# Kernel optimization log

Measured on AMD Instinct MI355X. Metric: run time of the kernel, lower is better.

## Reference

```python
import jax, jax.numpy as jnp
import numpy as np

BN_EPS = 1e-5


def ball_query(pos, radius, k):
    """PointNet++-style ball query: for each point, the first k point indices
    (in index order) whose distance < radius; shorter lists are padded with the
    first valid index (self is always valid since dist=0). pos: (b,n,3).
    Returns idx: (b,n,k) int32."""
    b, n, _ = pos.shape
    sq = jnp.sum(pos * pos, axis=-1)                       # (b,n)
    d2 = sq[:, :, None] + sq[:, None, :] - 2.0 * jnp.einsum('bnc,bmc->bnm', pos, pos)
    mask = d2 < radius * radius                            # (b,n,n)
    cand = jnp.where(mask, jnp.arange(n, dtype=jnp.int32)[None, None, :], jnp.int32(n))
    # smallest-k indices in ascending order == first-k valid in index order
    neg_top, _ = jax.lax.top_k(-cand, k)                   # (b,n,k)
    idx = -neg_top
    first = idx[..., :1]
    idx = jnp.where(idx == n, first, idx)                  # pad with first neighbor
    return idx


def reference(pos, x, w1, gamma, beta, w2, b2, radius, k):
    pos = jax.lax.stop_gradient(pos)
    idx = ball_query(pos, radius, k)                       # (b,n,k)
    grouped = jax.vmap(lambda p, i: p[i])(pos, idx)        # (b,n,k,3)
    rel = grouped - pos[:, :, None, :]                     # center-subtract
    # 1x1 conv (3->3, no bias)
    h = jnp.einsum('bnkc,dc->bnkd', rel, w1)
    # BatchNorm2d (training-mode batch stats over b,k,n per channel)
    mean = jnp.mean(h, axis=(0, 1, 2))
    var = jnp.mean((h - mean) ** 2, axis=(0, 1, 2))
    h = (h - mean) * jax.lax.rsqrt(var + BN_EPS) * gamma + beta
    h = jax.nn.relu(h)
    # 1x1 conv (3->out_channel) + bias
    pe = jnp.einsum('bnkd,ed->bnke', h, w2) + b2           # (b,n,k,C)
    pe = jnp.max(pe, axis=2)                               # max over k neighbors
    return x + pe


def setup_inputs() -> dict:
    key = jax.random.key(0)
    ks = jax.random.split(key, 5)
    b, n, c, kk = 2, 8192, 64, 32
    pos = jax.random.uniform(ks[0], (b, n, 3), dtype=jnp.float32)
    x = jax.random.normal(ks[1], (b, n, c), dtype=jnp.float32)
    w1 = jax.random.normal(ks[2], (3, 3), dtype=jnp.float32) * 0.5
    gamma = jnp.ones((3,), dtype=jnp.float32)
    beta = jnp.zeros((3,), dtype=jnp.float32)
    w2 = jax.random.normal(ks[3], (c, 3), dtype=jnp.float32) * 0.5
    b2 = jnp.zeros((c,), dtype=jnp.float32)
    radius = jnp.float32(0.1)
    return {"pos": pos, "x": x, "w1": w1, "gamma": gamma, "beta": beta,
            "w2": w2, "b2": b2, "radius": radius, "k": kk}
```

## Files before the change

kernel.cpp:

```cpp
#include <hip/hip_runtime.h>
#include <math.h>

#define NPTS   8192
#define NBATCH 2
#define NQ     (NPTS * NBATCH)
#define KNB    32
#define CFEAT  64
#define BN_EPS 1e-5f

#define MAXC     1000
#define CSTR     1024
#define CAP_HIT  128
#define CAP_CAND 640

#define QBK2  16
#define NBLK2 (NQ / QBK2)

#define WS_H    0
#define WS_PART (NQ * 3 * KNB)
#define WS_CS   (WS_PART + 6 * NBLK2)
#define WS_BIN  (WS_CS + 2 * CSTR)

__device__ __forceinline__ int grid_from_r(double rd) {
    int G = (int)(1.0 / rd);
    if (G < 1) G = 1;
    while (G > 1 && 1.0 / (double)G < rd) --G;
    if (G > 10) G = 10;
    return G;
}

__device__ __forceinline__ int mbcnt64(unsigned long long m) {
    return (int)__builtin_amdgcn_mbcnt_hi((unsigned)(m >> 32),
             __builtin_amdgcn_mbcnt_lo((unsigned)m, 0u));
}

__global__ __launch_bounds__(256) void kA_bin(
    const float* __restrict__ pos, const float* __restrict__ radius,
    float* __restrict__ ws)
{
    __shared__ int hist[MAXC];
    __shared__ int offs[MAXC + 1];
    __shared__ int cur[MAXC];
    __shared__ int scan[256];

    const int tid = threadIdx.x;
    const int batch = blockIdx.x;
    const float* bpos = pos + (size_t)batch * NPTS * 3;
    const double rd = (double)radius[0];
    const int G = grid_from_r(rd);
    const float Gf = (float)G;
    const int NC = G * G * G;

    for (int c = tid; c < NC; c += 256) hist[c] = 0;
    __syncthreads();
    for (int p = tid; p < NPTS; p += 256) {
        float x = bpos[p * 3], y = bpos[p * 3 + 1], z = bpos[p * 3 + 2];
        int cx = min((int)(x * Gf), G - 1);
        int cy = min((int)(y * Gf), G - 1);
        int cz = min((int)(z * Gf), G - 1);
        atomicAdd(&hist[(cz * G + cy) * G + cx], 1);
    }
    __syncthreads();

    const int CH = (MAXC + 255) / 256;
    const int base = tid * CH;
    int s = 0;
#pragma unroll
    for (int i = 0; i < CH; ++i) { int c = base + i; s += (c < NC) ? hist[c] : 0; }
    scan[tid] = s;
    __syncthreads();
    for (int off = 1; off < 256; off <<= 1) {
        int v = (tid >= off) ? scan[tid - off] : 0;
        __syncthreads();
        scan[tid] += v;
        __syncthreads();
    }
    int excl = (tid > 0) ? scan[tid - 1] : 0;
#pragma unroll
    for (int i = 0; i < CH; ++i) {
        int c = base + i;
        if (c < NC) { offs[c] = excl; excl += hist[c]; }
    }
    if (tid == 0) offs[NC] = NPTS;
    __syncthreads();
    for (int c = tid; c < NC; c += 256) cur[c] = offs[c];
    int* cs = (int*)ws + WS_CS + batch * CSTR;
    for (int c = tid; c <= NC; c += 256) cs[c] = offs[c];
    __syncthreads();

    float4* bin = (float4*)(ws + WS_BIN) + (size_t)batch * NPTS;
    for (int p = tid; p < NPTS; p += 256) {
        float x = bpos[p * 3], y = bpos[p * 3 + 1], z = bpos[p * 3 + 2];
        int cx = min((int)(x * Gf), G - 1);
        int cy = min((int)(y * Gf), G - 1);
        int cz = min((int)(z * Gf), G - 1);
        int slot = atomicAdd(&cur[(cz * G + cy) * G + cx], 1);
        bin[slot] = make_float4(x, y, z, __int_as_float(p));
    }
}

__global__ __launch_bounds__(256) void k2_query(
    const float* __restrict__ pos, const float* __restrict__ w1,
    const float* __restrict__ radius, float* __restrict__ ws)
{
    __shared__ int   candl[4][CAP_CAND];
    __shared__ int   hitl[QBK2][CAP_HIT];
    __shared__ int   seli[4][KNB];
    __shared__ float sred[4][6];

    const int tid = threadIdx.x, lane = tid & 63, wave = tid >> 6;
    const int qbase = blockIdx.x * QBK2;
    const int batch = qbase / NPTS;
    const float* bpos = pos + (size_t)batch * NPTS * 3;
    const double rd  = (double)radius[0];
    const double r2d = rd * rd;
    const int G = grid_from_r(rd);
    const float Gf = (float)G;
    const int* cs = (const int*)ws + WS_CS + batch * CSTR;
    const float4* bin = (const float4*)(ws + WS_BIN) + (size_t)batch * NPTS;

    float w1r[9];
#pragma unroll
    for (int i = 0; i < 9; ++i) w1r[i] = w1[i];

    float ls0 = 0.f, ls1 = 0.f, ls2 = 0.f;
    float lq0 = 0.f, lq1 = 0.f, lq2 = 0.f;

    for (int q = 0; q < 4; ++q) {
        const int qg = qbase + wave * 4 + q;
        const int ql = qg - batch * NPTS;
        const float qx = bpos[ql * 3], qy = bpos[ql * 3 + 1], qz = bpos[ql * 3 + 2];
        const double qxd = (double)qx, qyd = (double)qy, qzd = (double)qz;
        const double qsd = fma(qzd, qzd, fma(qyd, qyd, qxd * qxd));
        const int cx = min((int)(qx * Gf), G - 1);
        const int cy = min((int)(qy * Gf), G - 1);
        const int cz = min((int)(qz * Gf), G - 1);

        int cnt_l = 0, start_l = 0;
        if (lane < 27) {
            int dx = lane % 3 - 1, dy = (lane / 3) % 3 - 1, dz = lane / 9 - 1;
            int nx = cx + dx, ny = cy + dy, nz = cz + dz;
            if (nx >= 0 && nx < G && ny >= 0 && ny < G && nz >= 0 && nz < G) {
                int c = (nz * G + ny) * G + nx;
                start_l = cs[c];
                cnt_l = cs[c + 1] - start_l;
            }
        }
        int incl = cnt_l;
#pragma unroll
        for (int off = 1; off < 32; off <<= 1) {
            int v = __shfl_up(incl, off);
            if (lane >= off) incl += v;
        }
        int T = __shfl(incl, 26);
        if (T > CAP_CAND) T = CAP_CAND;
        const int pref = incl - cnt_l;
        if (lane < 27) {
            for (int t = 0; t < cnt_l; ++t) {
                int d = pref + t;
                if (d < CAP_CAND) candl[wave][d] = start_l + t;
            }
        }

        const int qs = wave * 4 + q;
        int hc = 0;
        for (int b0 = 0; b0 < T; b0 += 64) {
            int ss = b0 + lane;
            bool act = ss < T;
            int slot = act ? candl[wave][ss] : 0;
            float4 P = bin[slot];
            double xj = (double)P.x, yj = (double)P.y, zj = (double)P.z;
            double sqj = fma(zj, zj, fma(yj, yj, xj * xj));
            double dot = fma(zj, qzd, fma(yj, qyd, xj * qxd));
            double dd  = (qsd + sqj) - 2.0 * dot;
            bool in = act && (dd < r2d);
            unsigned long long bal = __ballot(in);
            if (in) {
                int p2 = hc + mbcnt64(bal);
                if (p2 < CAP_HIT) hitl[qs][p2] = __float_as_int(P.w);
            }
            hc += (int)__popcll(bal);
        }
        if (hc > CAP_HIT) hc = CAP_HIT;

        if (hc <= KNB) {
            int v = (lane < hc) ? hitl[qs][lane] : 0x7FFFFFFF;
            int mn = v;
#pragma unroll
            for (int off = 32; off; off >>= 1) mn = min(mn, __shfl_xor(mn, off));
            if (lane < KNB) seli[wave][lane] = (lane < hc) ? v : mn;
        } else {
            int a = (lane < hc) ? hitl[qs][lane] : 0x7FFFFFFF;
            int b = (64 + lane < hc) ? hitl[qs][64 + lane] : 0x7FFFFFFF;
            int lo = 0, hi = NPTS - 1;
            while (lo < hi) {
                int mid = (lo + hi) >> 1;
                int c1 = (int)__popcll(__ballot(a <= mid)) +
                         (int)__popcll(__ballot(b <= mid));
                if (c1 >= KNB) hi = mid; else lo = mid + 1;
            }
            const int t = lo;
            unsigned long long ba = __ballot(a <= t);
            unsigned long long bb = __ballot(b <= t);
            int na = (int)__popcll(ba);
            if (a <= t) seli[wave][mbcnt64(ba)] = a;
            if (b <= t) seli[wave][na + mbcnt64(bb)] = b;
        }

        if (lane < KNB) {
            int j = seli[wave][lane];
            const float* pj = bpos + (size_t)j * 3;
            float rx = __fsub_rn(pj[0], qx);
            float ry = __fsub_rn(pj[1], qy);
            float rz = __fsub_rn(pj[2], qz);
            float h0 = fmaf(rz, w1r[2], fmaf(ry, w1r[1], __fmul_rn(rx, w1r[0])));
            float h1 = fmaf(rz, w1r[5], fmaf(ry, w1r[4], __fmul_rn(rx, w1r[3])));
            float h2 = fmaf(rz, w1r[8], fmaf(ry, w1r[7], __fmul_rn(rx, w1r[6])));
            float* hout = ws + WS_H + (size_t)qg * 3 * KNB;
            hout[0 * KNB + lane] = h0;
            hout[1 * KNB + lane] = h1;
            hout[2 * KNB + lane] = h2;
            ls0 += h0; ls1 += h1; ls2 += h2;
            lq0 += h0 * h0; lq1 += h1 * h1; lq2 += h2 * h2;
        }
    }

#pragma unroll
    for (int m = 1; m < 64; m <<= 1) {
        ls0 += __shfl_xor(ls0, m); ls1 += __shfl_xor(ls1, m); ls2 += __shfl_xor(ls2, m);
        lq0 += __shfl_xor(lq0, m); lq1 += __shfl_xor(lq1, m); lq2 += __shfl_xor(lq2, m);
    }
    if (lane == 0) {
        sred[wave][0] = ls0; sred[wave][1] = ls1; sred[wave][2] = ls2;
        sred[wave][3] = lq0; sred[wave][4] = lq1; sred[wave][5] = lq2;
    }
    __syncthreads();
    if (tid == 0) {
#pragma unroll
        for (int c = 0; c < 6; ++c) {
            float s = sred[0][c] + sred[1][c] + sred[2][c] + sred[3][c];
            ws[WS_PART + c * NBLK2 + blockIdx.x] = s;
        }
    }
}

__global__ __launch_bounds__(256) void k3_mlp(
    const float* __restrict__ ws, const float* __restrict__ gamma,
    const float* __restrict__ beta, const float* __restrict__ w2,
    const float* __restrict__ b2, const float* __restrict__ x,
    float* __restrict__ out)
{
    __shared__ float wred[4][6];
    __shared__ float sstat[6];
    __shared__ float g[4][KNB][3];

    const int tid = threadIdx.x, lane = tid & 63, wave = tid >> 6;

#pragma unroll
    for (int c = 0; c < 6; ++c) {
        float s = 0.f;
        for (int i = tid; i < NBLK2; i += 256) s += ws[WS_PART + c * NBLK2 + i];
#pragma unroll
        for (int m = 1; m < 64; m <<= 1) s += __shfl_xor(s, m);
        if (lane == 0) wred[wave][c] = s;
    }
    __syncthreads();
    if (tid < 3) {
        const double N = (double)((long long)NQ * KNB);
        double s = 0.0, sq = 0.0;
#pragma unroll
        for (int w = 0; w < 4; ++w) { s += wred[w][tid]; sq += wred[w][3 + tid]; }
        double mean = s / N;
        double var  = sq / N - mean * mean;
        sstat[tid]     = (float)mean;
        sstat[3 + tid] = (float)(1.0 / sqrt(var + (double)BN_EPS));
    }
    __syncthreads();

    const float m0 = sstat[0], m1 = sstat[1], m2 = sstat[2];
    const float i0 = sstat[3], i1 = sstat[4], i2 = sstat[5];
    const float g0c = gamma[0], g1c = gamma[1], g2c = gamma[2];
    const float b0c = beta[0],  b1c = beta[1],  b2c = beta[2];
    const float w20 = w2[lane * 3 + 0];
    const float w21 = w2[lane * 3 + 1];
    const float w22 = w2[lane * 3 + 2];
    const float bias = b2[lane];

    const int qg0 = blockIdx.x * QBK2 + wave * 4;
#pragma unroll
    for (int q = 0; q < 4; ++q) {
        const int qg = qg0 + q;
        if (lane < KNB) {
            const float* hin = ws + WS_H + (size_t)qg * 3 * KNB;
            float h0 = hin[0 * KNB + lane];
            float h1 = hin[1 * KNB + lane];
            float h2 = hin[2 * KNB + lane];
            float n0 = __fadd_rn(__fmul_rn(__fmul_rn(__fsub_rn(h0, m0), i0), g0c), b0c);
            float n1 = __fadd_rn(__fmul_rn(__fmul_rn(__fsub_rn(h1, m1), i1), g1c), b1c);
            float n2 = __fadd_rn(__fmul_rn(__fmul_rn(__fsub_rn(h2, m2), i2), g2c), b2c);
            g[wave][lane][0] = fmaxf(n0, 0.0f);
            g[wave][lane][1] = fmaxf(n1, 0.0f);
            g[wave][lane][2] = fmaxf(n2, 0.0f);
        }
        __syncthreads();
        float m = -INFINITY;
#pragma unroll 4
        for (int kk = 0; kk < KNB; ++kk) {
            float ga = g[wave][kk][0], gb = g[wave][kk][1], gc = g[wave][kk][2];
            float pe = __fadd_rn(fmaf(gc, w22, fmaf(gb, w21, __fmul_rn(ga, w20))), bias);
            m = fmaxf(m, pe);
        }
        const size_t o = (size_t)qg * CFEAT + lane;
        out[o] = __fadd_rn(x[o], m);
        __syncthreads();
    }
}

extern "C" void kernel_launch(void* const* d_in, const int* in_sizes, int n_in,
                              void* d_out, int out_size, void* d_ws, size_t ws_size,
                              hipStream_t stream) {
    (void)in_sizes; (void)n_in; (void)out_size; (void)ws_size;
    const float* pos    = (const float*)d_in[0];
    const float* x      = (const float*)d_in[1];
    const float* w1     = (const float*)d_in[2];
    const float* gamma  = (const float*)d_in[3];
    const float* beta   = (const float*)d_in[4];
    const float* w2     = (const float*)d_in[5];
    const float* b2     = (const float*)d_in[6];
    const float* radius = (const float*)d_in[7];
    float* out = (float*)d_out;
    float* ws  = (float*)d_ws;

    hipLaunchKernelGGL(kA_bin,   dim3(NBATCH), dim3(256), 0, stream, pos, radius, ws);
    hipLaunchKernelGGL(k2_query, dim3(NBLK2),  dim3(256), 0, stream, pos, w1, radius, ws);
    hipLaunchKernelGGL(k3_mlp,   dim3(NBLK2),  dim3(256), 0, stream,
                       ws, gamma, beta, w2, b2, x, out);
}
```

Before: 69.67 us.

## Use one wave per query and scan contiguous cell rows without candidate list

The query kernel now runs 1024 threads per block so each of the 16 waves handles a single query instead of four queries per wave. It drops the shared-memory candidate list built from 27 cells and instead iterates 9 (y,z) rows, scanning the contiguous bin range that spans cx-1..cx+1 directly, since cells are stored x-fastest. The binning kernel also moves to 1024 threads with one cell per thread in the scan. These changes aim to cut serial per-wave work and the candidate-list staging, at the cost of larger blocks and more threads per point.

```diff
diff --git a/kernel.cpp b/kernel.cpp
--- a/kernel.cpp
+++ b/kernel.cpp
@@ -11,7 +11,6 @@
 #define MAXC     1000
 #define CSTR     1024
 #define CAP_HIT  128
-#define CAP_CAND 640
 
 #define QBK2  16
 #define NBLK2 (NQ / QBK2)
@@ -34,14 +33,14 @@
              __builtin_amdgcn_mbcnt_lo((unsigned)m, 0u));
 }
 
-__global__ __launch_bounds__(256) void kA_bin(
+__global__ __launch_bounds__(1024) void kA_bin(
     const float* __restrict__ pos, const float* __restrict__ radius,
     float* __restrict__ ws)
 {
     __shared__ int hist[MAXC];
     __shared__ int offs[MAXC + 1];
     __shared__ int cur[MAXC];
-    __shared__ int scan[256];
+    __shared__ int scan[1024];
 
     const int tid = threadIdx.x;
     const int batch = blockIdx.x;
@@ -51,9 +50,9 @@
     const float Gf = (float)G;
     const int NC = G * G * G;
 
-    for (int c = tid; c < NC; c += 256) hist[c] = 0;
-    __syncthreads();
-    for (int p = tid; p < NPTS; p += 256) {
+    for (int c = tid; c < NC; c += 1024) hist[c] = 0;
+    __syncthreads();
+    for (int p = tid; p < NPTS; p += 1024) {
         float x = bpos[p * 3], y = bpos[p * 3 + 1], z = bpos[p * 3 + 2];
         int cx = min((int)(x * Gf), G - 1);
         int cy = min((int)(y * Gf), G - 1);
@@ -62,34 +61,27 @@
     }
     __syncthreads();
 
-    const int CH = (MAXC + 255) / 256;
-    const int base = tid * CH;
-    int s = 0;
-#pragma unroll
-    for (int i = 0; i < CH; ++i) { int c = base + i; s += (c < NC) ? hist[c] : 0; }
-    scan[tid] = s;
-    __syncthreads();
-    for (int off = 1; off < 256; off <<= 1) {
-        int v = (tid >= off) ? scan[tid - off] : 0;
+    int v = (tid < NC) ? hist[tid] : 0;
+    scan[tid] = v;
+    __syncthreads();
+    for (int off = 1; off < 1024; off <<= 1) {
+        int t = (tid >= off) ? scan[tid - off] : 0;
         __syncthreads();
-        scan[tid] += v;
+        scan[tid] += t;
         __syncthreads();
     }
-    int excl = (tid > 0) ? scan[tid - 1] : 0;
-#pragma unroll
-    for (int i = 0; i < CH; ++i) {
-        int c = base + i;
-        if (c < NC) { offs[c] = excl; excl += hist[c]; }
+    if (tid < NC) {
+        int excl = (tid > 0) ? scan[tid - 1] : 0;
+        offs[tid] = excl;
+        cur[tid]  = excl;
     }
     if (tid == 0) offs[NC] = NPTS;
     __syncthreads();
-    for (int c = tid; c < NC; c += 256) cur[c] = offs[c];
     int* cs = (int*)ws + WS_CS + batch * CSTR;
-    for (int c = tid; c <= NC; c += 256) cs[c] = offs[c];
-    __syncthreads();
+    for (int c = tid; c <= NC; c += 1024) cs[c] = offs[c];
 
     float4* bin = (float4*)(ws + WS_BIN) + (size_t)batch * NPTS;
-    for (int p = tid; p < NPTS; p += 256) {
+    for (int p = tid; p < NPTS; p += 1024) {
         float x = bpos[p * 3], y = bpos[p * 3 + 1], z = bpos[p * 3 + 2];
         int cx = min((int)(x * Gf), G - 1);
         int cy = min((int)(y * Gf), G - 1);
@@ -99,14 +91,13 @@
     }
 }
 
-__global__ __launch_bounds__(256) void k2_query(
+__global__ __launch_bounds__(1024) void k2_query(
     const float* __restrict__ pos, const float* __restrict__ w1,
     const float* __restrict__ radius, float* __restrict__ ws)
 {
-    __shared__ int   candl[4][CAP_CAND];
     __shared__ int   hitl[QBK2][CAP_HIT];
-    __shared__ int   seli[4][KNB];
-    __shared__ float sred[4][6];
+    __shared__ int   seli[QBK2][KNB];
+    __shared__ float sred[QBK2][6];
 
     const int tid = threadIdx.x, lane = tid & 63, wave = tid >> 6;
     const int qbase = blockIdx.x * QBK2;
@@ -119,56 +110,29 @@
     const int* cs = (const int*)ws + WS_CS + batch * CSTR;
     const float4* bin = (const float4*)(ws + WS_BIN) + (size_t)batch * NPTS;
 
-    float w1r[9];
-#pragma unroll
-    for (int i = 0; i < 9; ++i) w1r[i] = w1[i];
-
-    float ls0 = 0.f, ls1 = 0.f, ls2 = 0.f;
-    float lq0 = 0.f, lq1 = 0.f, lq2 = 0.f;
-
-    for (int q = 0; q < 4; ++q) {
-        const int qg = qbase + wave * 4 + q;
-        const int ql = qg - batch * NPTS;
-        const float qx = bpos[ql * 3], qy = bpos[ql * 3 + 1], qz = bpos[ql * 3 + 2];
-        const double qxd = (double)qx, qyd = (double)qy, qzd = (double)qz;
-        const double qsd = fma(qzd, qzd, fma(qyd, qyd, qxd * qxd));
-        const int cx = min((int)(qx * Gf), G - 1);
-        const int cy = min((int)(qy * Gf), G - 1);
-        const int cz = min((int)(qz * Gf), G - 1);
-
-        int cnt_l = 0, start_l = 0;
-        if (lane < 27) {
-            int dx = lane % 3 - 1, dy = (lane / 3) % 3 - 1, dz = lane / 9 - 1;
-            int nx = cx + dx, ny = cy + dy, nz = cz + dz;
-            if (nx >= 0 && nx < G && ny >= 0 && ny < G && nz >= 0 && nz < G) {
-                int c = (nz * G + ny) * G + nx;
-                start_l = cs[c];
-                cnt_l = cs[c + 1] - start_l;
-            }
-        }
-        int incl = cnt_l;
-#pragma unroll
-        for (int off = 1; off < 32; off <<= 1) {
-            int v = __shfl_up(incl, off);
-            if (lane >= off) incl += v;
-        }
-        int T = __shfl(incl, 26);
-        if (T > CAP_CAND) T = CAP_CAND;
-        const int pref = incl - cnt_l;
-        if (lane < 27) {
-            for (int t = 0; t < cnt_l; ++t) {
-                int d = pref + t;
-                if (d < CAP_CAND) candl[wave][d] = start_l + t;
-            }
-        }
-
-        const int qs = wave * 4 + q;
-        int hc = 0;
-        for (int b0 = 0; b0 < T; b0 += 64) {
-            int ss = b0 + lane;
-            bool act = ss < T;
-            int slot = act ? candl[wave][ss] : 0;
-            float4 P = bin[slot];
+    const int qg = qbase + wave;
+    const int ql = qg - batch * NPTS;
+    const float qx = bpos[ql * 3], qy = bpos[ql * 3 + 1], qz = bpos[ql * 3 + 2];
+    const double qxd = (double)qx, qyd = (double)qy, qzd = (double)qz;
+    const double qsd = fma(qzd, qzd, fma(qyd, qyd, qxd * qxd));
+    const int cx = min((int)(qx * Gf), G - 1);
+    const int cy = min((int)(qy * Gf), G - 1);
+    const int cz = min((int)(qz * Gf), G - 1);
+    const int cx0 = max(cx - 1, 0), cx1 = min(cx + 1, G - 1);
+
+    int hc = 0;
+#pragma unroll
+    for (int r = 0; r < 9; ++r) {
+        const int ny = cy + (r % 3) - 1;
+        const int nz = cz + (r / 3) - 1;
+        if (ny < 0 || ny >= G || nz < 0 || nz >= G) continue;
+        const int cb = (nz * G + ny) * G;
+        const int s0 = cs[cb + cx0];
+        const int s1 = cs[cb + cx1 + 1];
+        for (int b0 = s0; b0 < s1; b0 += 64) {
+            const int ss = b0 + lane;
+            const bool act = ss < s1;
+            float4 P = bin[act ? ss : s0];
             double xj = (double)P.x, yj = (double)P.y, zj = (double)P.z;
             double sqj = fma(zj, zj, fma(yj, yj, xj * xj));
             double dot = fma(zj, qzd, fma(yj, qyd, xj * qxd));
@@ -177,52 +141,58 @@
             unsigned long long bal = __ballot(in);
             if (in) {
                 int p2 = hc + mbcnt64(bal);
-                if (p2 < CAP_HIT) hitl[qs][p2] = __float_as_int(P.w);
+                if (p2 < CAP_HIT) hitl[wave][p2] = __float_as_int(P.w);
             }
             hc += (int)__popcll(bal);
         }
-        if (hc > CAP_HIT) hc = CAP_HIT;
-
-        if (hc <= KNB) {
-            int v = (lane < hc) ? hitl[qs][lane] : 0x7FFFFFFF;
-            int mn = v;
-#pragma unroll
-            for (int off = 32; off; off >>= 1) mn = min(mn, __shfl_xor(mn, off));
-            if (lane < KNB) seli[wave][lane] = (lane < hc) ? v : mn;
-        } else {
-            int a = (lane < hc) ? hitl[qs][lane] : 0x7FFFFFFF;
-            int b = (64 + lane < hc) ? hitl[qs][64 + lane] : 0x7FFFFFFF;
-            int lo = 0, hi = NPTS - 1;
-            while (lo < hi) {
-                int mid = (lo + hi) >> 1;
-                int c1 = (int)__popcll(__ballot(a <= mid)) +
-                         (int)__popcll(__ballot(b <= mid));
-                if (c1 >= KNB) hi = mid; else lo = mid + 1;
-            }
-            const int t = lo;
-            unsigned long long ba = __ballot(a <= t);
-            unsigned long long bb = __ballot(b <= t);
-            int na = (int)__popcll(ba);
-            if (a <= t) seli[wave][mbcnt64(ba)] = a;
-            if (b <= t) seli[wave][na + mbcnt64(bb)] = b;
+    }
+    if (hc > CAP_HIT) hc = CAP_HIT;
+
+    if (hc <= KNB) {
+        int v = (lane < hc) ? hitl[wave][lane] : 0x7FFFFFFF;
+        int mn = v;
+#pragma unroll
+        for (int off = 32; off; off >>= 1) mn = min(mn, __shfl_xor(mn, off));
+        if (lane < KNB) seli[wave][lane] = (lane < hc) ? v : mn;
+    } else {
+        int a = (lane < hc) ? hitl[wave][lane] : 0x7FFFFFFF;
+        int b = (64 + lane < hc) ? hitl[wave][64 + lane] : 0x7FFFFFFF;
+        int lo = 0, hi = NPTS - 1;
+        while (lo < hi) {
+            int mid = (lo + hi) >> 1;
+            int c1 = (int)__popcll(__ballot(a <= mid)) +
+                     (int)__popcll(__ballot(b <= mid));
+            if (c1 >= KNB) hi = mid; else lo = mid + 1;
         }
-
-        if (lane < KNB) {
-            int j = seli[wave][lane];
-            const float* pj = bpos + (size_t)j * 3;
-            float rx = __fsub_rn(pj[0], qx);
-            float ry = __fsub_rn(pj[1], qy);
-            float rz = __fsub_rn(pj[2], qz);
-            float h0 = fmaf(rz, w1r[2], fmaf(ry, w1r[1], __fmul_rn(rx, w1r[0])));
-            float h1 = fmaf(rz, w1r[5], fmaf(ry, w1r[4], __fmul_rn(rx, w1r[3])));
-            float h2 = fmaf(rz, w1r[8], fmaf(ry, w1r[7], __fmul_rn(rx, w1r[6])));
-            float* hout = ws + WS_H + (size_t)qg * 3 * KNB;
-            hout[0 * KNB + lane] = h0;
-            hout[1 * KNB + lane] = h1;
-            hout[2 * KNB + lane] = h2;
-            ls0 += h0; ls1 += h1; ls2 += h2;
-            lq0 += h0 * h0; lq1 += h1 * h1; lq2 += h2 * h2;
-        }
+        const int t = lo;
+        unsigned long long ba = __ballot(a <= t);
+        unsigned long long bb = __ballot(b <= t);
+        int na = (int)__popcll(ba);
+        if (a <= t) seli[wave][mbcnt64(ba)] = a;
+        if (b <= t) seli[wave][na + mbcnt64(bb)] = b;
+    }
+
+    float w1r[9];
+#pragma unroll
+    for (int i = 0; i < 9; ++i) w1r[i] = w1[i];
+
+    float ls0 = 0.f, ls1 = 0.f, ls2 = 0.f;
+    float lq0 = 0.f, lq1 = 0.f, lq2 = 0.f;
+    if (lane < KNB) {
+        int j = seli[wave][lane];
+        const float* pj = bpos + (size_t)j * 3;
+        float rx = __fsub_rn(pj[0], qx);
+        float ry = __fsub_rn(pj[1], qy);
+        float rz = __fsub_rn(pj[2], qz);
+        float h0 = fmaf(rz, w1r[2], fmaf(ry, w1r[1], __fmul_rn(rx, w1r[0])));
+        float h1 = fmaf(rz, w1r[5], fmaf(ry, w1r[4], __fmul_rn(rx, w1r[3])));
+        float h2 = fmaf(rz, w1r[8], fmaf(ry, w1r[7], __fmul_rn(rx, w1r[6])));
+        float* hout = ws + WS_H + (size_t)qg * 3 * KNB;
+        hout[0 * KNB + lane] = h0;
+        hout[1 * KNB + lane] = h1;
+        hout[2 * KNB + lane] = h2;
+        ls0 = h0; ls1 = h1; ls2 = h2;
+        lq0 = h0 * h0; lq1 = h1 * h1; lq2 = h2 * h2;
     }
 
 #pragma unroll
@@ -235,12 +205,11 @@
         sred[wave][3] = lq0; sred[wave][4] = lq1; sred[wave][5] = lq2;
     }
     __syncthreads();
-    if (tid == 0) {
-#pragma unroll
-        for (int c = 0; c < 6; ++c) {
-            float s = sred[0][c] + sred[1][c] + sred[2][c] + sred[3][c];
-            ws[WS_PART + c * NBLK2 + blockIdx.x] = s;
-        }
+    if (tid < 6) {
+        float s = 0.f;
+#pragma unroll
+        for (int w = 0; w < QBK2; ++w) s += sred[w][tid];
+        ws[WS_PART + tid * NBLK2 + blockIdx.x] = s;
     }
 }
 
@@ -331,8 +300,8 @@
     float* out = (float*)d_out;
     float* ws  = (float*)d_ws;
 
-    hipLaunchKernelGGL(kA_bin,   dim3(NBATCH), dim3(256), 0, stream, pos, radius, ws);
-    hipLaunchKernelGGL(k2_query, dim3(NBLK2),  dim3(256), 0, stream, pos, w1, radius, ws);
-    hipLaunchKernelGGL(k3_mlp,   dim3(NBLK2),  dim3(256), 0, stream,
+    hipLaunchKernelGGL(kA_bin,   dim3(NBATCH), dim3(1024), 0, stream, pos, radius, ws);
+    hipLaunchKernelGGL(k2_query, dim3(NBLK2),  dim3(1024), 0, stream, pos, w1, radius, ws);
+    hipLaunchKernelGGL(k3_mlp,   dim3(NBLK2),  dim3(256),  0, stream,
                        ws, gamma, beta, w2, b2, x, out);
 }
```

Result: faster. 63.40 us (-9.0%).
